# Optimization experiments

Measured on AMD Instinct MI355X. Metric: run time of the kernel, lower is better.

The kernel has to match this reference:

```python
import jax, jax.numpy as jnp
import numpy as np

N = 100000   # nodes
E = 2000000  # edges per etype
D = 256      # in_dim
C = 16       # num_classes (per-etype Linear out dim)
R = 4        # number of canonical etypes


def setup_inputs() -> dict:
    key = jax.random.key(0)
    k0, k1, k2, k3, k4, k5 = jax.random.split(key, 6)
    feat = jax.random.normal(k0, (N, D), dtype=jnp.float32)
    src_idx = jax.random.randint(k1, (R, E), 0, N, dtype=jnp.int32)
    dst_idx = jax.random.randint(k2, (R, E), 0, N, dtype=jnp.int32)
    eweight = jax.random.uniform(k3, (R, E, 1), dtype=jnp.float32)
    W = jax.random.normal(k4, (R, D, C), dtype=jnp.float32) / np.sqrt(D).astype(np.float32)
    b = jax.random.normal(k5, (R, C), dtype=jnp.float32) * 0.01
    return {"feat": feat, "src_idx": src_idx, "dst_idx": dst_idx,
            "eweight": eweight, "W": W, "b": b}


def reference(feat, src_idx, dst_idx, eweight, W, b):
    """Hetero GNN layer: per-etype Linear -> u_mul_e message -> mean reduce per
    dst node -> sum across etypes (DGL multi_update_all(..., 'sum'))."""
    n = feat.shape[0]

    def per_etype(Wr, br, src, dst, ew):
        wh = feat @ Wr + br                      # [N, C] per-etype linear
        m = jnp.take(wh, src, axis=0) * ew       # [E, C] u_mul_e message
        s = jax.ops.segment_sum(m, dst, num_segments=n)            # [N, C]
        cnt = jax.ops.segment_sum(jnp.ones((src.shape[0],), feat.dtype),
                                  dst, num_segments=n)             # [N]
        # DGL mean: nodes with no incoming messages contribute 0
        cnt = cnt[:, None]
        return jnp.where(cnt > 0, s / jnp.maximum(cnt, 1.0), jnp.zeros_like(s))

    h = jax.vmap(per_etype)(W, b, src_idx, dst_idx, eweight)  # [R, N, C]
    return h.sum(axis=0)                                       # cross-etype sum
```

## Files before the change

### kernel.cpp

```cpp
#include <hip/hip_runtime.h>

constexpr int N = 100000;
constexpr int E = 2000000;
constexpr int D = 256;
constexpr int C = 16;
constexpr int R = 4;
constexpr int NCOL = R * C;
constexpr int TOT = R * E;

constexpr int BKN = 256;
constexpr int NBUK = (N + BKN - 1) / BKN;
constexpr int EPB = 16384;
constexpr int NBLK = (E + EPB - 1) / EPB;
constexpr int NROWS = R * NBUK;
constexpr int HLEN = NROWS * NBLK;
constexpr int SCAN_ELEMS = 2048;
constexpr int SCAN_NBLK = (HLEN + SCAN_ELEMS - 1) / SCAN_ELEMS;
constexpr int CAP = 6144;
constexpr int CHK = 4096;

typedef __attribute__((ext_vector_type(8))) short short8;
typedef __attribute__((ext_vector_type(4))) float f32x4;
typedef __attribute__((ext_vector_type(4))) int i32x4;

__device__ __forceinline__ float bf2f(unsigned short h) {
    return __uint_as_float(((unsigned int)h) << 16);
}
__device__ __forceinline__ unsigned short f2bf(float f) {
    unsigned int x = __float_as_uint(f);
    x += 0x7FFFu + ((x >> 16) & 1u);
    return (unsigned short)(x >> 16);
}

__global__ void wt_kernel(const float* __restrict__ W, short8* __restrict__ wtb) {
    const int idx = blockIdx.x * blockDim.x + threadIdx.x;
    if (idx >= 8 * 4 * 64) return;
    const int lane = idx & 63;
    const int ct   = (idx >> 6) & 3;
    const int ks   = idx >> 8;
    const int r = ct, c = lane & 15;
    const int kbase = ks * 32 + (lane >> 4) * 8;
    short8 v;
#pragma unroll
    for (int j = 0; j < 8; ++j)
        v[j] = (short)f2bf(W[(size_t)r * D * C + (size_t)(kbase + j) * C + c]);
    wtb[idx] = v;
}

__global__ __launch_bounds__(256) void gemm_kernel(
    const f32x4* __restrict__ feat4, const short8* __restrict__ wtb,
    const float* __restrict__ b, unsigned short* __restrict__ whb) {
    __shared__ unsigned short alds[64 * 272];
    const int t   = threadIdx.x;
    const int n0  = blockIdx.x * 64;

#pragma unroll
    for (int j = 0; j < 16; ++j) {
        const int idx = t + j * 256;
        const int row = idx >> 6, k4 = idx & 63;
        const int grow = n0 + row;
        const int lrow = (grow < N) ? grow : (N - 1);
        const f32x4 v = __builtin_nontemporal_load(&feat4[(size_t)lrow * 64 + k4]);
        ushort4 u;
        u.x = f2bf(v.x); u.y = f2bf(v.y); u.z = f2bf(v.z); u.w = f2bf(v.w);
        *(ushort4*)&alds[row * 272 + k4 * 4] = u;
    }
    __syncthreads();

    const int lane = t & 63;
    const int wv   = t >> 6;
    const int wrow = wv * 16 + (lane & 15);
    const int kblk = lane >> 4;

    f32x4 acc0 = {0.f, 0.f, 0.f, 0.f};
    f32x4 acc1 = acc0, acc2 = acc0, acc3 = acc0;

#pragma unroll
    for (int ks = 0; ks < 8; ++ks) {
        const short8 af = *(const short8*)&alds[wrow * 272 + ks * 32 + kblk * 8];
        const short8 b0 = wtb[(ks * 4 + 0) * 64 + lane];
        const short8 b1 = wtb[(ks * 4 + 1) * 64 + lane];
        const short8 b2 = wtb[(ks * 4 + 2) * 64 + lane];
        const short8 b3 = wtb[(ks * 4 + 3) * 64 + lane];
        acc0 = __builtin_amdgcn_mfma_f32_16x16x32_bf16(af, b0, acc0, 0, 0, 0);
        acc1 = __builtin_amdgcn_mfma_f32_16x16x32_bf16(af, b1, acc1, 0, 0, 0);
        acc2 = __builtin_amdgcn_mfma_f32_16x16x32_bf16(af, b2, acc2, 0, 0, 0);
        acc3 = __builtin_amdgcn_mfma_f32_16x16x32_bf16(af, b3, acc3, 0, 0, 0);
    }

    const int c    = lane & 15;
    const int rowb = n0 + wv * 16 + (lane >> 4) * 4;
    const float bias0 = b[ 0 + c];
    const float bias1 = b[16 + c];
    const float bias2 = b[32 + c];
    const float bias3 = b[48 + c];
#pragma unroll
    for (int reg = 0; reg < 4; ++reg) {
        const int gr = rowb + reg;
        if (gr < N) {
            whb[((size_t)0 * N + gr) * 16 + c] = f2bf(acc0[reg] + bias0);
            whb[((size_t)1 * N + gr) * 16 + c] = f2bf(acc1[reg] + bias1);
            whb[((size_t)2 * N + gr) * 16 + c] = f2bf(acc2[reg] + bias2);
            whb[((size_t)3 * N + gr) * 16 + c] = f2bf(acc3[reg] + bias3);
        }
    }
}

__global__ __launch_bounds__(256) void hist_kernel(const int* __restrict__ dst,
                                                   int* __restrict__ hist) {
    __shared__ int hcnt[NBUK];
    const int t = threadIdx.x;
    const int r = blockIdx.y;
    for (int i = t; i < NBUK; i += 256) hcnt[i] = 0;
    __syncthreads();
    const int e0 = blockIdx.x * EPB;
    if (E - e0 >= EPB) {
        const i32x4* d4 = (const i32x4*)(dst + (size_t)r * E + e0);
#pragma unroll
        for (int j = 0; j < EPB / 1024; ++j) {
            const i32x4 d = __builtin_nontemporal_load(&d4[t + j * 256]);
            atomicAdd(&hcnt[d.x >> 8], 1);
            atomicAdd(&hcnt[d.y >> 8], 1);
            atomicAdd(&hcnt[d.z >> 8], 1);
            atomicAdd(&hcnt[d.w >> 8], 1);
        }
    } else {
        const int* d = dst + (size_t)r * E;
        for (int e = e0 + t; e < E; e += 256)
            atomicAdd(&hcnt[d[e] >> 8], 1);
    }
    __syncthreads();
    for (int i = t; i < NBUK; i += 256)
        hist[(size_t)(r * NBUK + i) * NBLK + blockIdx.x] = hcnt[i];
}

__global__ __launch_bounds__(256) void scan1_kernel(int* __restrict__ data,
                                                    int* __restrict__ partials) {
    __shared__ int sh[256];
    const int t = threadIdx.x;
    const int idx = blockIdx.x * SCAN_ELEMS + t * 8;
    int v[8];
#pragma unroll
    for (int j = 0; j < 8; ++j)
        v[j] = (idx + j < HLEN) ? data[idx + j] : 0;
    int s = 0;
#pragma unroll
    for (int j = 0; j < 8; ++j) s += v[j];
    sh[t] = s;
    __syncthreads();
    for (int off = 1; off < 256; off <<= 1) {
        int x = (t >= off) ? sh[t - off] : 0;
        __syncthreads();
        sh[t] += x;
        __syncthreads();
    }
    int run = sh[t] - s;
    if (t == 255) partials[blockIdx.x] = sh[255];
#pragma unroll
    for (int j = 0; j < 8; ++j) {
        if (idx + j < HLEN) data[idx + j] = run;
        run += v[j];
    }
}

__global__ __launch_bounds__(1024) void scan2_kernel(int* __restrict__ partials, int n) {
    __shared__ int sh[1024];
    const int t = threadIdx.x;
    int a = (2 * t     < n) ? partials[2 * t]     : 0;
    int b = (2 * t + 1 < n) ? partials[2 * t + 1] : 0;
    const int s = a + b;
    sh[t] = s;
    __syncthreads();
    for (int off = 1; off < 1024; off <<= 1) {
        int x = (t >= off) ? sh[t - off] : 0;
        __syncthreads();
        sh[t] += x;
        __syncthreads();
    }
    const int excl = sh[t] - s;
    if (2 * t     < n) partials[2 * t]     = excl;
    if (2 * t + 1 < n) partials[2 * t + 1] = excl + a;
}

__global__ void scan3_kernel(int* __restrict__ data, const int* __restrict__ partials) {
    const int i = blockIdx.x * blockDim.x + threadIdx.x;
    if (i < HLEN) data[i] += partials[i / SCAN_ELEMS];
}

__global__ __launch_bounds__(512) void scatter_kernel(const int* __restrict__ src,
                                                      const int* __restrict__ dst,
                                                      const float* __restrict__ ew,
                                                      const int* __restrict__ hist,
                                                      int2* __restrict__ sorted) {
    __shared__ int2 lrec[CHK];
    __shared__ int  lidx[CHK];
    __shared__ short lbkt[CHK];
    __shared__ int gcur[NBUK];
    __shared__ int loff[NBUK + 1];
    __shared__ int lcnt[NBUK];
    const int t = threadIdx.x;
    const int r = blockIdx.y;

    for (int i = t; i < NBUK; i += 512)
        gcur[i] = hist[(size_t)(r * NBUK + i) * NBLK + blockIdx.x];

    const int e0 = blockIdx.x * EPB;
    const int e1 = min(e0 + EPB, E);
    const int* sp = src + (size_t)r * E;
    const int* dp = dst + (size_t)r * E;
    const float* wp = ew + (size_t)r * E;

    for (int cb = e0; cb < e1; cb += CHK) {
        const int L = min(CHK, e1 - cb);
        for (int i = t; i < NBUK; i += 512) lcnt[i] = 0;
        __syncthreads();

        if (L == CHK) {
            const i32x4* s4 = (const i32x4*)(sp + cb);
            const i32x4* d4 = (const i32x4*)(dp + cb);
            const f32x4* w4 = (const f32x4*)(wp + cb);
#pragma unroll
            for (int j = 0; j < CHK / 2048; ++j) {
                const int v = t + j * 512;
                const i32x4 d = __builtin_nontemporal_load(&d4[v]);
                const i32x4 s = __builtin_nontemporal_load(&s4[v]);
                const f32x4 w = __builtin_nontemporal_load(&w4[v]);
#pragma unroll
                for (int q = 0; q < 4; ++q) {
                    const int dd = (q == 0) ? d.x : (q == 1) ? d.y : (q == 2) ? d.z : d.w;
                    const int ss = (q == 0) ? s.x : (q == 1) ? s.y : (q == 2) ? s.z : s.w;
                    const float ww = (q == 0) ? w.x : (q == 1) ? w.y : (q == 2) ? w.z : w.w;
                    const int b = dd >> 8;
                    int2 p;
                    p.x = ss | ((dd & 255) << 20);
                    p.y = __float_as_int(ww);
                    lrec[v * 4 + q] = p;
                    lbkt[v * 4 + q] = (short)b;
                    atomicAdd(&lcnt[b], 1);
                }
            }
        } else {
            for (int i = t; i < L; i += 512) {
                const int dd = dp[cb + i];
                const int ss = sp[cb + i];
                const float ww = wp[cb + i];
                const int b = dd >> 8;
                int2 p;
                p.x = ss | ((dd & 255) << 20);
                p.y = __float_as_int(ww);
                lrec[i] = p;
                lbkt[i] = (short)b;
                atomicAdd(&lcnt[b], 1);
            }
        }
        __syncthreads();

        for (int off = 1; off < NBUK; off <<= 1) {
            int x = 0;
            if (t < NBUK && t >= off) x = lcnt[t - off];
            __syncthreads();
            if (t < NBUK) lcnt[t] += x;
            __syncthreads();
        }
        if (t < NBUK) loff[t + 1] = lcnt[t];
        if (t == 0) loff[0] = 0;
        __syncthreads();
        if (t < NBUK) lcnt[t] = loff[t];
        __syncthreads();

        for (int i = t; i < L; i += 512) {
            const int b = lbkt[i];
            const int pos = atomicAdd(&lcnt[b], 1);
            lidx[pos] = i | (b << 16);
        }
        __syncthreads();

        for (int p = t; p < L; p += 512) {
            const int v = lidx[p];
            const int i = v & 0xFFFF;
            const int b = v >> 16;
            sorted[gcur[b] + (p - loff[b])] = lrec[i];
        }
        __syncthreads();

        for (int b = t; b < NBUK; b += 512)
            gcur[b] += loff[b + 1] - loff[b];
        __syncthreads();
    }
}

__global__ __launch_bounds__(512) void accum_kernel(const int2* __restrict__ sorted,
                                                    const ushort4* __restrict__ whb4,
                                                    const int* __restrict__ hist,
                                                    float* __restrict__ part) {
    __shared__ int2 lrec[CAP];
    __shared__ int loff[BKN + 1];
    __shared__ int lcur[BKN];
    const int t = threadIdx.x;
    const int ck = blockIdx.x;
    const int r  = blockIdx.y;
    const int g = t >> 2, c4 = t & 3;

    const int row = r * NBUK + ck;
    const int start = hist[(size_t)row * NBLK];
    const int end   = (row + 1 < NROWS) ? hist[(size_t)(row + 1) * NBLK] : TOT;
    int L = end - start;
    if (L > CAP) L = CAP;

    if (t < BKN) lcur[t] = 0;
    __syncthreads();

    for (int i = t; i < L; i += 512)
        atomicAdd(&lcur[(sorted[start + i].x >> 20) & 255], 1);
    __syncthreads();

    for (int off = 1; off < BKN; off <<= 1) {
        int x = 0;
        if (t < BKN && t >= off) x = lcur[t - off];
        __syncthreads();
        if (t < BKN) lcur[t] += x;
        __syncthreads();
    }
    if (t < BKN) loff[t + 1] = lcur[t];
    if (t == 0) loff[0] = 0;
    __syncthreads();
    if (t < BKN) lcur[t] = loff[t];
    __syncthreads();

    for (int i = t; i < L; i += 512) {
        const int2 p = sorted[start + i];
        const int dl = (p.x >> 20) & 255;
        const int pos = atomicAdd(&lcur[dl], 1);
        lrec[pos] = p;
    }
    __syncthreads();

    const int wbase = r * N;
    float4 ov[2];
#pragma unroll
    for (int half = 0; half < 2; ++half) {
        const int node = g + half * 128;
        const int s0 = loff[node], e0 = loff[node + 1];
        float a0 = 0.f, a1 = 0.f, a2 = 0.f, a3 = 0.f;

        int j = s0;
        for (; j + 4 <= e0; j += 4) {
            const int2 r0 = lrec[j], r1 = lrec[j + 1];
            const int2 r2 = lrec[j + 2], r3 = lrec[j + 3];
            const ushort4 u0 = whb4[(size_t)(wbase + (r0.x & 0xFFFFF)) * 4 + c4];
            const ushort4 u1 = whb4[(size_t)(wbase + (r1.x & 0xFFFFF)) * 4 + c4];
            const ushort4 u2 = whb4[(size_t)(wbase + (r2.x & 0xFFFFF)) * 4 + c4];
            const ushort4 u3 = whb4[(size_t)(wbase + (r3.x & 0xFFFFF)) * 4 + c4];
            const float w0 = __int_as_float(r0.y), w1 = __int_as_float(r1.y);
            const float w2 = __int_as_float(r2.y), w3 = __int_as_float(r3.y);
            a0 += bf2f(u0.x) * w0 + bf2f(u1.x) * w1 + bf2f(u2.x) * w2 + bf2f(u3.x) * w3;
            a1 += bf2f(u0.y) * w0 + bf2f(u1.y) * w1 + bf2f(u2.y) * w2 + bf2f(u3.y) * w3;
            a2 += bf2f(u0.z) * w0 + bf2f(u1.z) * w1 + bf2f(u2.z) * w2 + bf2f(u3.z) * w3;
            a3 += bf2f(u0.w) * w0 + bf2f(u1.w) * w1 + bf2f(u2.w) * w2 + bf2f(u3.w) * w3;
        }
        for (; j < e0; ++j) {
            const int2 r0 = lrec[j];
            const ushort4 u0 = whb4[(size_t)(wbase + (r0.x & 0xFFFFF)) * 4 + c4];
            const float w0 = __int_as_float(r0.y);
            a0 += bf2f(u0.x) * w0;
            a1 += bf2f(u0.y) * w0;
            a2 += bf2f(u0.z) * w0;
            a3 += bf2f(u0.w) * w0;
        }

        const int deg = e0 - s0;
        const float inv = (deg > 0) ? 1.f / (float)deg : 0.f;
        ov[half].x = a0 * inv; ov[half].y = a1 * inv;
        ov[half].z = a2 * inv; ov[half].w = a3 * inv;
    }

    const int nodeA = ck * BKN + g;
    const int nodeB = nodeA + 128;
    if (nodeA < N) *(float4*)&part[(size_t)(wbase + nodeA) * 16 + c4 * 4] = ov[0];
    if (nodeB < N) *(float4*)&part[(size_t)(wbase + nodeB) * 16 + c4 * 4] = ov[1];
}

__global__ void finalize_kernel(const float4* __restrict__ part4,
                                float4* __restrict__ out4) {
    const int i = blockIdx.x * blockDim.x + threadIdx.x;
    if (i >= N * 4) return;
    float4 a = part4[i];
    const float4 b = part4[(size_t)N * 4 + i];
    const float4 c = part4[(size_t)2 * N * 4 + i];
    const float4 d = part4[(size_t)3 * N * 4 + i];
    a.x += b.x + c.x + d.x;
    a.y += b.y + c.y + d.y;
    a.z += b.z + c.z + d.z;
    a.w += b.w + c.w + d.w;
    out4[i] = a;
}

extern "C" void kernel_launch(void* const* d_in, const int* in_sizes, int n_in,
                              void* d_out, int out_size, void* d_ws, size_t ws_size,
                              hipStream_t stream) {
    const float* feat = (const float*)d_in[0];
    const int*   src  = (const int*)d_in[1];
    const int*   dst  = (const int*)d_in[2];
    const float* ew   = (const float*)d_in[3];
    const float* W    = (const float*)d_in[4];
    const float* b    = (const float*)d_in[5];
    float* out = (float*)d_out;

    char* base = (char*)d_ws;
    int2*           sorted   = (int2*)base;           base += (size_t)TOT * 8;
    short8*         wtb      = (short8*)base;         base += (size_t)64 * NCOL * 16;
    unsigned short* whb      = (unsigned short*)base; base += (size_t)R * N * C * 2;
    int*            hist     = (int*)base;            base += (size_t)HLEN * 4;
    int*            partials = (int*)base;            base += (size_t)4096;
    float*          part     = (float*)base;

    wt_kernel<<<8, 256, 0, stream>>>(W, wtb);
    gemm_kernel<<<(N + 63) / 64, 256, 0, stream>>>((const f32x4*)feat, wtb, b, whb);

    hist_kernel<<<dim3(NBLK, R), 256, 0, stream>>>(dst, hist);
    scan1_kernel<<<SCAN_NBLK, 256, 0, stream>>>(hist, partials);
    scan2_kernel<<<1, 1024, 0, stream>>>(partials, SCAN_NBLK);
    scan3_kernel<<<(HLEN + 255) / 256, 256, 0, stream>>>(hist, partials);

    scatter_kernel<<<dim3(NBLK, R), 512, 0, stream>>>(src, dst, ew, hist, sorted);
    accum_kernel<<<dim3(NBUK, R), 512, 0, stream>>>(sorted, (const ushort4*)whb, hist, part);
    finalize_kernel<<<(N * 4 + 255) / 256, 256, 0, stream>>>((const float4*)part, (float4*)out);
}
```

Baseline: 186.4 us.

## Stage bucket records once in LDS and gather wider rows with two threads per node

```diff
diff --git a/kernel.cpp b/kernel.cpp
--- a/kernel.cpp
+++ b/kernel.cpp
@@ -20,6 +20,7 @@
 constexpr int CHK = 4096;
 
 typedef __attribute__((ext_vector_type(8))) short short8;
+typedef __attribute__((ext_vector_type(8))) unsigned short u16x8;
 typedef __attribute__((ext_vector_type(4))) float f32x4;
 typedef __attribute__((ext_vector_type(4))) int i32x4;
 
@@ -290,16 +291,17 @@
 }
 
 __global__ __launch_bounds__(512) void accum_kernel(const int2* __restrict__ sorted,
-                                                    const ushort4* __restrict__ whb4,
+                                                    const u16x8* __restrict__ whb8,
                                                     const int* __restrict__ hist,
                                                     float* __restrict__ part) {
     __shared__ int2 lrec[CAP];
+    __shared__ unsigned short lidx[CAP];
     __shared__ int loff[BKN + 1];
     __shared__ int lcur[BKN];
     const int t = threadIdx.x;
     const int ck = blockIdx.x;
     const int r  = blockIdx.y;
-    const int g = t >> 2, c4 = t & 3;
+    const int g = t >> 1, h = t & 1;
 
     const int row = r * NBUK + ck;
     const int start = hist[(size_t)row * NBLK];
@@ -310,8 +312,12 @@
     if (t < BKN) lcur[t] = 0;
     __syncthreads();
 
-    for (int i = t; i < L; i += 512)
-        atomicAdd(&lcur[(sorted[start + i].x >> 20) & 255], 1);
+    for (int i = t; i < L; i += 512) {
+        long long raw = __builtin_nontemporal_load((const long long*)&sorted[start + i]);
+        int2 p = *(int2*)&raw;
+        lrec[i] = p;
+        atomicAdd(&lcur[(p.x >> 20) & 255], 1);
+    }
     __syncthreads();
 
     for (int off = 1; off < BKN; off <<= 1) {
@@ -328,56 +334,58 @@
     __syncthreads();
 
     for (int i = t; i < L; i += 512) {
-        const int2 p = sorted[start + i];
-        const int dl = (p.x >> 20) & 255;
+        const int dl = (lrec[i].x >> 20) & 255;
         const int pos = atomicAdd(&lcur[dl], 1);
-        lrec[pos] = p;
+        lidx[pos] = (unsigned short)i;
     }
     __syncthreads();
 
     const int wbase = r * N;
-    float4 ov[2];
-#pragma unroll
-    for (int half = 0; half < 2; ++half) {
-        const int node = g + half * 128;
-        const int s0 = loff[node], e0 = loff[node + 1];
-        float a0 = 0.f, a1 = 0.f, a2 = 0.f, a3 = 0.f;
-
-        int j = s0;
-        for (; j + 4 <= e0; j += 4) {
-            const int2 r0 = lrec[j], r1 = lrec[j + 1];
-            const int2 r2 = lrec[j + 2], r3 = lrec[j + 3];
-            const ushort4 u0 = whb4[(size_t)(wbase + (r0.x & 0xFFFFF)) * 4 + c4];
-            const ushort4 u1 = whb4[(size_t)(wbase + (r1.x & 0xFFFFF)) * 4 + c4];
-            const ushort4 u2 = whb4[(size_t)(wbase + (r2.x & 0xFFFFF)) * 4 + c4];
-            const ushort4 u3 = whb4[(size_t)(wbase + (r3.x & 0xFFFFF)) * 4 + c4];
-            const float w0 = __int_as_float(r0.y), w1 = __int_as_float(r1.y);
-            const float w2 = __int_as_float(r2.y), w3 = __int_as_float(r3.y);
-            a0 += bf2f(u0.x) * w0 + bf2f(u1.x) * w1 + bf2f(u2.x) * w2 + bf2f(u3.x) * w3;
-            a1 += bf2f(u0.y) * w0 + bf2f(u1.y) * w1 + bf2f(u2.y) * w2 + bf2f(u3.y) * w3;
-            a2 += bf2f(u0.z) * w0 + bf2f(u1.z) * w1 + bf2f(u2.z) * w2 + bf2f(u3.z) * w3;
-            a3 += bf2f(u0.w) * w0 + bf2f(u1.w) * w1 + bf2f(u2.w) * w2 + bf2f(u3.w) * w3;
-        }
-        for (; j < e0; ++j) {
-            const int2 r0 = lrec[j];
-            const ushort4 u0 = whb4[(size_t)(wbase + (r0.x & 0xFFFFF)) * 4 + c4];
-            const float w0 = __int_as_float(r0.y);
-            a0 += bf2f(u0.x) * w0;
-            a1 += bf2f(u0.y) * w0;
-            a2 += bf2f(u0.z) * w0;
-            a3 += bf2f(u0.w) * w0;
-        }
-
+    const int s0 = loff[g], e0 = loff[g + 1];
+    float a0 = 0.f, a1 = 0.f, a2 = 0.f, a3 = 0.f;
+    float a4 = 0.f, a5 = 0.f, a6 = 0.f, a7 = 0.f;
+
+    int j = s0;
+    for (; j + 4 <= e0; j += 4) {
+        const int i0 = lidx[j], i1 = lidx[j + 1];
+        const int i2 = lidx[j + 2], i3 = lidx[j + 3];
+        const int2 r0 = lrec[i0], r1 = lrec[i1], r2 = lrec[i2], r3 = lrec[i3];
+        const u16x8 u0 = whb8[(size_t)(wbase + (r0.x & 0xFFFFF)) * 2 + h];
+        const u16x8 u1 = whb8[(size_t)(wbase + (r1.x & 0xFFFFF)) * 2 + h];
+        const u16x8 u2 = whb8[(size_t)(wbase + (r2.x & 0xFFFFF)) * 2 + h];
+        const u16x8 u3 = whb8[(size_t)(wbase + (r3.x & 0xFFFFF)) * 2 + h];
+        const float w0 = __int_as_float(r0.y), w1 = __int_as_float(r1.y);
+        const float w2 = __int_as_float(r2.y), w3 = __int_as_float(r3.y);
+        a0 += bf2f(u0[0]) * w0 + bf2f(u1[0]) * w1 + bf2f(u2[0]) * w2 + bf2f(u3[0]) * w3;
+        a1 += bf2f(u0[1]) * w0 + bf2f(u1[1]) * w1 + bf2f(u2[1]) * w2 + bf2f(u3[1]) * w3;
+        a2 += bf2f(u0[2]) * w0 + bf2f(u1[2]) * w1 + bf2f(u2[2]) * w2 + bf2f(u3[2]) * w3;
+        a3 += bf2f(u0[3]) * w0 + bf2f(u1[3]) * w1 + bf2f(u2[3]) * w2 + bf2f(u3[3]) * w3;
+        a4 += bf2f(u0[4]) * w0 + bf2f(u1[4]) * w1 + bf2f(u2[4]) * w2 + bf2f(u3[4]) * w3;
+        a5 += bf2f(u0[5]) * w0 + bf2f(u1[5]) * w1 + bf2f(u2[5]) * w2 + bf2f(u3[5]) * w3;
+        a6 += bf2f(u0[6]) * w0 + bf2f(u1[6]) * w1 + bf2f(u2[6]) * w2 + bf2f(u3[6]) * w3;
+        a7 += bf2f(u0[7]) * w0 + bf2f(u1[7]) * w1 + bf2f(u2[7]) * w2 + bf2f(u3[7]) * w3;
+    }
+    for (; j < e0; ++j) {
+        const int2 r0 = lrec[lidx[j]];
+        const u16x8 u0 = whb8[(size_t)(wbase + (r0.x & 0xFFFFF)) * 2 + h];
+        const float w0 = __int_as_float(r0.y);
+        a0 += bf2f(u0[0]) * w0; a1 += bf2f(u0[1]) * w0;
+        a2 += bf2f(u0[2]) * w0; a3 += bf2f(u0[3]) * w0;
+        a4 += bf2f(u0[4]) * w0; a5 += bf2f(u0[5]) * w0;
+        a6 += bf2f(u0[6]) * w0; a7 += bf2f(u0[7]) * w0;
+    }
+
+    const int node = ck * BKN + g;
+    if (node < N) {
         const int deg = e0 - s0;
         const float inv = (deg > 0) ? 1.f / (float)deg : 0.f;
-        ov[half].x = a0 * inv; ov[half].y = a1 * inv;
-        ov[half].z = a2 * inv; ov[half].w = a3 * inv;
-    }
-
-    const int nodeA = ck * BKN + g;
-    const int nodeB = nodeA + 128;
-    if (nodeA < N) *(float4*)&part[(size_t)(wbase + nodeA) * 16 + c4 * 4] = ov[0];
-    if (nodeB < N) *(float4*)&part[(size_t)(wbase + nodeB) * 16 + c4 * 4] = ov[1];
+        float4 v0, v1;
+        v0.x = a0 * inv; v0.y = a1 * inv; v0.z = a2 * inv; v0.w = a3 * inv;
+        v1.x = a4 * inv; v1.y = a5 * inv; v1.z = a6 * inv; v1.w = a7 * inv;
+        float* op = &part[(size_t)(wbase + node) * 16 + h * 8];
+        *(float4*)op = v0;
+        *(float4*)(op + 4) = v1;
+    }
 }
 
 __global__ void finalize_kernel(const float4* __restrict__ part4,
@@ -423,6 +431,6 @@
     scan3_kernel<<<(HLEN + 255) / 256, 256, 0, stream>>>(hist, partials);
 
     scatter_kernel<<<dim3(NBLK, R), 512, 0, stream>>>(src, dst, ew, hist, sorted);
-    accum_kernel<<<dim3(NBUK, R), 512, 0, stream>>>(sorted, (const ushort4*)whb, hist, part);
+    accum_kernel<<<dim3(NBUK, R), 512, 0, stream>>>(sorted, (const u16x8*)whb, hist, part);
     finalize_kernel<<<(N * 4 + 255) / 256, 256, 0, stream>>>((const float4*)part, (float4*)out);
 }
```

Measured after the change: 188.6 us. About the same (+1.2%).
